# Performance work log

Measured on AMD Instinct MI355X. Metric: run time of the kernel, lower is better.

The kernel has to match this reference:

```python
import jax, jax.numpy as jnp
import numpy as np

T, IO, H, M = 8192, 32, 256, 4  # timesteps, io_width, hidden_width, max ponder steps
EPS = 0.01  # ACT halting epsilon


def setup_inputs() -> dict:
    key = jax.random.key(0)
    ks = jax.random.split(key, 8)
    sc = 0.05
    return {
        "x": jax.random.normal(ks[0], (T, IO), jnp.float32),
        "h0": jnp.zeros((H,), jnp.float32),                       # act1_h initial state
        "Wp": jax.random.normal(ks[1], (H, IO), jnp.float32) * sc,  # input_processing Linear
        "bp": jnp.zeros((H,), jnp.float32),
        "Wx": jax.random.normal(ks[2], (H, H + 1), jnp.float32) * sc,  # ACT cell input weights (+1 first-step flag)
        "Ws": jax.random.normal(ks[3], (H, H), jnp.float32) * sc,      # ACT cell recurrent weights
        "b": jnp.zeros((H,), jnp.float32),
        "wh": jax.random.normal(ks[4], (H,), jnp.float32) * sc,        # halting unit
        "bh": jnp.float32(1.0),
        "Wo": jax.random.normal(ks[5], (IO, H), jnp.float32) * sc,     # ACT output projection
        "bo": jnp.zeros((IO,), jnp.float32),
    }


def reference(x, h0, Wp, bp, Wx, Ws, b, wh, bh, Wo, bo):
    # Faithful translation: per-timestep loop (lax.scan) over the sequence; each step
    # runs input_processing then an ACT (Graves) ponder loop with max M=4 steps.
    # io_noise is identity in eval mode. attention_beam_width=1 => line == current point.
    T_ = x.shape[0]

    def step(carry, x_t):
        h, pc = carry
        lin1 = Wp @ x_t + bp  # [H]
        s = h
        cum = jnp.float32(0.0)
        acc_s = jnp.zeros_like(h)
        acc_y = jnp.zeros_like(bo)
        n_up = jnp.float32(0.0)
        rem = jnp.float32(0.0)
        still = jnp.bool_(True)
        for n in range(M):  # fixed small ponder loop, masked ACT halting
            flag = jnp.full((1,), 1.0 if n == 0 else 0.0, lin1.dtype)
            inp = jnp.concatenate([lin1, flag])  # [H+1]
            s = jnp.tanh(Wx @ inp + Ws @ s + b)
            p = jax.nn.sigmoid(wh @ s + bh)
            halt = (cum + p > 1.0 - EPS) | (n == M - 1)
            w = jnp.where(still, jnp.where(halt, 1.0 - cum, p), 0.0)
            acc_s = acc_s + w * s
            acc_y = acc_y + w * (Wo @ s + bo)
            rem = rem + jnp.where(still & halt, 1.0 - cum, 0.0)
            n_up = n_up + jnp.where(still, 1.0, 0.0)
            cum = cum + w
            still = still & jnp.logical_not(halt)
        ponder = n_up + rem  # N(t) + R(t)
        pc = (pc + ponder) / jnp.float32(T_)  # matches the in-loop division in the original forward
        return (acc_s, pc), acc_y

    (_, pc), ys = jax.lax.scan(step, (h0, jnp.float32(0.0)), x)
    return ys, pc
```

## Files before the change

kernel.cpp:

```cpp
#include <hip/hip_runtime.h>


#define T_  8192
#define IO_ 32
#define H_  256

template<int CTRL>
__device__ __forceinline__ float dpp_addf(float x) {
    int xi = __builtin_bit_cast(int, x);
    int d = __builtin_amdgcn_update_dpp(xi, xi, CTRL, 0xF, 0xF, false);
    return x + __builtin_bit_cast(float, d);
}

__global__ void k_prep(const float* __restrict__ Wx,
                       const float* __restrict__ Wp,
                       const float* __restrict__ bp,
                       const float* __restrict__ b,
                       float* __restrict__ WxpT, float* __restrict__ cvec) {
    int h = blockIdx.x;
    int t = threadIdx.x;
    __shared__ float wxrow[H_];
    for (int j = t; j < H_; j += 64) wxrow[j] = Wx[h * (H_ + 1) + j];
    __syncthreads();
    if (t < IO_) {
        float acc = 0.0f;
        for (int j = 0; j < H_; ++j) acc += wxrow[j] * Wp[j * IO_ + t];
        WxpT[t * H_ + h] = acc;
    } else if (t == IO_) {
        float acc = b[h];
        for (int j = 0; j < H_; ++j) acc += wxrow[j] * bp[j];
        cvec[h] = acc;
    }
}

__global__ void k_u(const float* __restrict__ x,
                    const float* __restrict__ WxpT,
                    const float* __restrict__ cvec,
                    float* __restrict__ U) {
    int t0 = blockIdx.x * 8;
    int tid = threadIdx.x;
    __shared__ float xsf[8 * IO_];
    xsf[tid] = x[(size_t)t0 * IO_ + tid];
    __syncthreads();
    int h = tid;
    float base = cvec[h];
    for (int tt = 0; tt < 8; ++tt) {
        float acc = base;
        #pragma unroll
        for (int io = 0; io < IO_; ++io)
            acc += WxpT[io * H_ + h] * xsf[tt * IO_ + io];
        U[(size_t)(t0 + tt) * H_ + h] = acc;
    }
}

__global__ __launch_bounds__(512, 2) void act_chain(
    const float* __restrict__ Ws,
    const float* __restrict__ Wx,
    const float* __restrict__ wh,
    const float* __restrict__ bh1,
    const float* __restrict__ h0,
    float* __restrict__ UAcc,
    float* __restrict__ cumArr,
    float* __restrict__ pc_out)
{
    __shared__ __align__(16) float sbuf[2][288];
    __shared__ __align__(16) float plds[2][8];

    const int tid = threadIdx.x;
    const int w   = tid >> 6;
    const int l   = tid & 63;
    const int rg  = l >> 3;
    const int c   = l & 7;
    const int rowbase = w * 32 + rg * 4;

    float4 wq[4][8];
    #pragma unroll
    for (int r = 0; r < 4; ++r) {
        const float4* src = (const float4*)(Ws + (size_t)(rowbase + r) * H_ + c * 32);
        #pragma unroll
        for (int k = 0; k < 8; ++k) wq[r][k] = src[k];
    }

    float wl4[4], whv4[4];
    #pragma unroll
    for (int r = 0; r < 4; ++r) {
        wl4[r]  = Wx[(size_t)(rowbase + r) * (H_ + 1) + H_];
        whv4[r] = wh[rowbase + r];
    }
    const float bhf = bh1[0];
    const float thresh = 1.0f - 0.01f;

    if (tid < H_) sbuf[0][(tid >> 5) * 36 + (tid & 31)] = h0[tid];
    __syncthreads();

    int cur = 0, pp = 0;
    float pc = 0.0f;

    #pragma unroll 1
    for (int tg = 0; tg < T_ / 4; ++tg) {
        float4 un[4];
        #pragma unroll
        for (int k = 0; k < 4; ++k)
            un[k] = *(const float4*)(UAcc + (size_t)(tg * 4 + k) * H_ + rowbase);

        float4 av[4];
        float  cu4[4];

        #pragma unroll
        for (int k = 0; k < 4; ++k) {
            const float u0 = un[k].x, u1 = un[k].y, u2 = un[k].z, u3 = un[k].w;

            float accs[4] = {0.f, 0.f, 0.f, 0.f};
            float cum = 0.0f, nup = 0.0f, remt = 0.0f;
            float sn[4];

            #pragma unroll 1
            for (int n = 0; n < 4; ++n) {
                const float4* sp = (const float4*)(&sbuf[cur][c * 36]);
                float4 sv[8];
                #pragma unroll
                for (int q = 0; q < 8; ++q) sv[q] = sp[q];

                float y[4];
                #pragma unroll
                for (int r = 0; r < 4; ++r) {
                    float a = 0.0f;
                    #pragma unroll
                    for (int q = 0; q < 8; ++q) {
                        a += wq[r][q].x * sv[q].x;
                        a += wq[r][q].y * sv[q].y;
                        a += wq[r][q].z * sv[q].z;
                        a += wq[r][q].w * sv[q].w;
                    }
                    a = dpp_addf<0xB1>(a);
                    a = dpp_addf<0x4E>(a);
                    a = dpp_addf<0x141>(a);
                    y[r] = a;
                }

                float part = 0.0f;
                float uu[4] = {u0, u1, u2, u3};
                #pragma unroll
                for (int r = 0; r < 4; ++r) {
                    float yy = y[r] + uu[r] + ((n == 0) ? wl4[r] : 0.0f);
                    float e = __expf(2.0f * yy);
                    sn[r] = 1.0f - 2.0f * __builtin_amdgcn_rcpf(e + 1.0f);
                    part += whv4[r] * sn[r];
                }

                int nxt = cur ^ 1;
                if (c == 0)
                    *(float4*)(&sbuf[nxt][w * 36 + rg * 4]) =
                        make_float4(sn[0], sn[1], sn[2], sn[3]);

                part = dpp_addf<0x128>(part);
                part = dpp_addf<0x142>(part);
                part = dpp_addf<0x143>(part);
                if (l == 63) plds[pp][w] = part;
                __syncthreads();

                float4 pa = *(const float4*)(&plds[pp][0]);
                float4 pb = *(const float4*)(&plds[pp][4]);
                float dot = ((pa.x + pa.y) + (pa.z + pa.w)) +
                            ((pb.x + pb.y) + (pb.z + pb.w));
                pp ^= 1;
                float p = __builtin_amdgcn_rcpf(1.0f + __expf(-(dot + bhf)));
                bool halt = (cum + p > thresh) || (n == 3);
                float hw = 1.0f - cum;
                float wn = halt ? hw : p;
                #pragma unroll
                for (int r = 0; r < 4; ++r) accs[r] += wn * sn[r];
                nup += 1.0f;
                cum += wn;
                if (halt) { remt = hw; break; }
                cur = nxt;
            }

            pc = (pc + nup + remt) * (1.0f / (float)T_);

            int hb = cur ^ 1;
            av[k] = make_float4(accs[0], accs[1], accs[2], accs[3]);
            cu4[k] = cum;
            if (c == 0)
                *(float4*)(&sbuf[hb][w * 36 + rg * 4]) = av[k];
            cur = hb;
            __syncthreads();
        }

        if (c == 0) {
            #pragma unroll
            for (int k = 0; k < 4; ++k)
                *(float4*)(UAcc + (size_t)(tg * 4 + k) * H_ + rowbase) = av[k];
        }
        if (tid == 0) {
            #pragma unroll
            for (int k = 0; k < 4; ++k) cumArr[tg * 4 + k] = cu4[k];
        }
    }
    if (tid == 0) pc_out[0] = pc;
}

__global__ void k_out(const float* __restrict__ AccS,
                      const float* __restrict__ Wo,
                      const float* __restrict__ bo,
                      const float* __restrict__ cumArr,
                      float* __restrict__ ys) {
    int t0 = blockIdx.x * 8;
    int tid = threadIdx.x;
    __shared__ float wo[IO_ * 257];
    __shared__ float as[8 * 260];
    for (int i = tid; i < IO_ * H_; i += 256) {
        int o = i / H_, h = i % H_;
        wo[o * 257 + h] = Wo[i];
    }
    for (int i = tid; i < 8 * H_; i += 256) {
        int tt = i / H_, h = i % H_;
        as[tt * 260 + h] = AccS[(size_t)t0 * H_ + i];
    }
    __syncthreads();
    int tt = tid >> 5, o = tid & 31;
    float acc = cumArr[t0 + tt] * bo[o];
    #pragma unroll 4
    for (int h = 0; h < H_; ++h) acc += wo[o * 257 + h] * as[tt * 260 + h];
    ys[(size_t)(t0 + tt) * IO_ + o] = acc;
}

extern "C" void kernel_launch(void* const* d_in, const int* in_sizes, int n_in,
                              void* d_out, int out_size, void* d_ws, size_t ws_size,
                              hipStream_t stream) {
    const float* x  = (const float*)d_in[0];
    const float* h0 = (const float*)d_in[1];
    const float* Wp = (const float*)d_in[2];
    const float* bp = (const float*)d_in[3];
    const float* Wx = (const float*)d_in[4];
    const float* Ws = (const float*)d_in[5];
    const float* b  = (const float*)d_in[6];
    const float* wh = (const float*)d_in[7];
    const float* bh = (const float*)d_in[8];
    const float* Wo = (const float*)d_in[9];
    const float* bo = (const float*)d_in[10];
    float* out = (float*)d_out;

    char* ws = (char*)d_ws;
    float* WxpT = (float*)ws;
    float* cvec = (float*)(ws + 32768);
    float* cumA = (float*)(ws + 33792);
    float* UAcc = (float*)(ws + 66560);

    k_prep<<<H_, 64, 0, stream>>>(Wx, Wp, bp, b, WxpT, cvec);
    k_u<<<T_ / 8, 256, 0, stream>>>(x, WxpT, cvec, UAcc);
    act_chain<<<1, 512, 0, stream>>>(Ws, Wx, wh, bh, h0, UAcc, cumA,
                                     out + (size_t)T_ * IO_);
    k_out<<<T_ / 8, 256, 0, stream>>>(UAcc, Wo, bo, cumA, out);
}
```

Before: 14.75 ms.

## Remap recurrent matvec to 2 rows x 4 column chunks with packed FP32 FMAs

Reworks the work split of the serial ACT chain kernel: each lane now owns 2 rows and a 64-column chunk (4 lanes per row group) instead of 4 rows and a 32-column chunk. The dot products use 2-wide float vectors so the compiler can emit packed FMA instructions. The cross-lane reduction shrinks to two DPP steps, while the halting-unit reduction gains one. The shared state buffer layout is changed to match. The tanh and sigmoid now call exp2 directly with prescaled constants. The aim is to shorten the per-ponder-step latency of the single-block recurrence, at the cost of longer per-lane accumulation chains and a different LDS read pattern.

```diff
diff --git a/kernel.cpp b/kernel.cpp
--- a/kernel.cpp
+++ b/kernel.cpp
@@ -4,6 +4,8 @@
 #define T_  8192
 #define IO_ 32
 #define H_  256
+
+typedef __attribute__((ext_vector_type(2))) float v2f;
 
 template<int CTRL>
 __device__ __forceinline__ float dpp_addf(float x) {
@@ -63,34 +65,41 @@
     float* __restrict__ cumArr,
     float* __restrict__ pc_out)
 {
-    __shared__ __align__(16) float sbuf[2][288];
+    __shared__ __align__(16) float sbuf[2][4 * 68];
     __shared__ __align__(16) float plds[2][8];
 
     const int tid = threadIdx.x;
     const int w   = tid >> 6;
     const int l   = tid & 63;
-    const int rg  = l >> 3;
-    const int c   = l & 7;
-    const int rowbase = w * 32 + rg * 4;
-
-    float4 wq[4][8];
+    const int rg  = l >> 2;
+    const int c   = l & 3;
+    const int rowbase = w * 32 + rg * 2;
+    const int schunk  = rowbase >> 6;
+    const int soff    = rowbase & 63;
+
+    v2f wt[2][32];
     #pragma unroll
-    for (int r = 0; r < 4; ++r) {
-        const float4* src = (const float4*)(Ws + (size_t)(rowbase + r) * H_ + c * 32);
-        #pragma unroll
-        for (int k = 0; k < 8; ++k) wq[r][k] = src[k];
-    }
-
-    float wl4[4], whv4[4];
-    #pragma unroll
-    for (int r = 0; r < 4; ++r) {
-        wl4[r]  = Wx[(size_t)(rowbase + r) * (H_ + 1) + H_];
-        whv4[r] = wh[rowbase + r];
-    }
+    for (int r = 0; r < 2; ++r) {
+        const float4* src = (const float4*)(Ws + (size_t)(rowbase + r) * H_ + c * 64);
+        #pragma unroll
+        for (int q = 0; q < 16; ++q) {
+            float4 f = src[q];
+            wt[r][2 * q]     = (v2f){f.x, f.y};
+            wt[r][2 * q + 1] = (v2f){f.z, f.w};
+        }
+    }
+
+    v2f wl2, whv2;
+    wl2.x  = Wx[(size_t)rowbase * (H_ + 1) + H_];
+    wl2.y  = Wx[(size_t)(rowbase + 1) * (H_ + 1) + H_];
+    whv2.x = wh[rowbase];
+    whv2.y = wh[rowbase + 1];
     const float bhf = bh1[0];
     const float thresh = 1.0f - 0.01f;
-
-    if (tid < H_) sbuf[0][(tid >> 5) * 36 + (tid & 31)] = h0[tid];
+    const float L2E  = 1.4426950408889634f;
+    const float L2E2 = 2.8853900817779268f;
+
+    if (tid < H_) sbuf[0][(tid >> 6) * 68 + (tid & 63)] = h0[tid];
     __syncthreads();
 
     int cur = 0, pp = 0;
@@ -98,61 +107,56 @@
 
     #pragma unroll 1
     for (int tg = 0; tg < T_ / 4; ++tg) {
-        float4 un[4];
+        v2f un[4];
         #pragma unroll
         for (int k = 0; k < 4; ++k)
-            un[k] = *(const float4*)(UAcc + (size_t)(tg * 4 + k) * H_ + rowbase);
-
-        float4 av[4];
-        float  cu4[4];
+            un[k] = *(const v2f*)(UAcc + (size_t)(tg * 4 + k) * H_ + rowbase);
+
+        v2f   av[4];
+        float cu4[4];
 
         #pragma unroll
         for (int k = 0; k < 4; ++k) {
-            const float u0 = un[k].x, u1 = un[k].y, u2 = un[k].z, u3 = un[k].w;
-
-            float accs[4] = {0.f, 0.f, 0.f, 0.f};
+            const v2f uu1 = un[k];
+            const v2f uu0 = uu1 + wl2;
+
+            v2f accs = {0.f, 0.f};
             float cum = 0.0f, nup = 0.0f, remt = 0.0f;
-            float sn[4];
+            float sn0, sn1;
 
             #pragma unroll 1
             for (int n = 0; n < 4; ++n) {
-                const float4* sp = (const float4*)(&sbuf[cur][c * 36]);
-                float4 sv[8];
+                v2f acc0 = {0.f, 0.f}, acc1 = {0.f, 0.f};
+                const float4* sp = (const float4*)(&sbuf[cur][c * 68]);
                 #pragma unroll
-                for (int q = 0; q < 8; ++q) sv[q] = sp[q];
-
-                float y[4];
-                #pragma unroll
-                for (int r = 0; r < 4; ++r) {
-                    float a = 0.0f;
-                    #pragma unroll
-                    for (int q = 0; q < 8; ++q) {
-                        a += wq[r][q].x * sv[q].x;
-                        a += wq[r][q].y * sv[q].y;
-                        a += wq[r][q].z * sv[q].z;
-                        a += wq[r][q].w * sv[q].w;
-                    }
-                    a = dpp_addf<0xB1>(a);
-                    a = dpp_addf<0x4E>(a);
-                    a = dpp_addf<0x141>(a);
-                    y[r] = a;
+                for (int q = 0; q < 16; ++q) {
+                    float4 f = sp[q];
+                    v2f sa = (v2f){f.x, f.y};
+                    v2f sb = (v2f){f.z, f.w};
+                    acc0 = acc0 + wt[0][2 * q] * sa;
+                    acc0 = acc0 + wt[0][2 * q + 1] * sb;
+                    acc1 = acc1 + wt[1][2 * q] * sa;
+                    acc1 = acc1 + wt[1][2 * q + 1] * sb;
                 }
-
-                float part = 0.0f;
-                float uu[4] = {u0, u1, u2, u3};
-                #pragma unroll
-                for (int r = 0; r < 4; ++r) {
-                    float yy = y[r] + uu[r] + ((n == 0) ? wl4[r] : 0.0f);
-                    float e = __expf(2.0f * yy);
-                    sn[r] = 1.0f - 2.0f * __builtin_amdgcn_rcpf(e + 1.0f);
-                    part += whv4[r] * sn[r];
-                }
+                float y0 = acc0.x + acc0.y;
+                float y1 = acc1.x + acc1.y;
+                y0 = dpp_addf<0xB1>(y0); y0 = dpp_addf<0x4E>(y0);
+                y1 = dpp_addf<0xB1>(y1); y1 = dpp_addf<0x4E>(y1);
+
+                v2f uu = (n == 0) ? uu0 : uu1;
+                float yy0 = y0 + uu.x;
+                float yy1 = y1 + uu.y;
+                float e0 = __builtin_amdgcn_exp2f(yy0 * L2E2);
+                float e1 = __builtin_amdgcn_exp2f(yy1 * L2E2);
+                sn0 = __builtin_fmaf(-2.0f, __builtin_amdgcn_rcpf(e0 + 1.0f), 1.0f);
+                sn1 = __builtin_fmaf(-2.0f, __builtin_amdgcn_rcpf(e1 + 1.0f), 1.0f);
 
                 int nxt = cur ^ 1;
                 if (c == 0)
-                    *(float4*)(&sbuf[nxt][w * 36 + rg * 4]) =
-                        make_float4(sn[0], sn[1], sn[2], sn[3]);
-
+                    *(v2f*)(&sbuf[nxt][schunk * 68 + soff]) = (v2f){sn0, sn1};
+
+                float part = __builtin_fmaf(whv2.x, sn0, whv2.y * sn1);
+                part = dpp_addf<0x124>(part);
                 part = dpp_addf<0x128>(part);
                 part = dpp_addf<0x142>(part);
                 part = dpp_addf<0x143>(part);
@@ -164,12 +168,12 @@
                 float dot = ((pa.x + pa.y) + (pa.z + pa.w)) +
                             ((pb.x + pb.y) + (pb.z + pb.w));
                 pp ^= 1;
-                float p = __builtin_amdgcn_rcpf(1.0f + __expf(-(dot + bhf)));
+                float p = __builtin_amdgcn_rcpf(
+                    1.0f + __builtin_amdgcn_exp2f(-(dot + bhf) * L2E));
                 bool halt = (cum + p > thresh) || (n == 3);
                 float hw = 1.0f - cum;
                 float wn = halt ? hw : p;
-                #pragma unroll
-                for (int r = 0; r < 4; ++r) accs[r] += wn * sn[r];
+                accs = accs + wn * (v2f){sn0, sn1};
                 nup += 1.0f;
                 cum += wn;
                 if (halt) { remt = hw; break; }
@@ -179,10 +183,10 @@
             pc = (pc + nup + remt) * (1.0f / (float)T_);
 
             int hb = cur ^ 1;
-            av[k] = make_float4(accs[0], accs[1], accs[2], accs[3]);
+            av[k]  = accs;
             cu4[k] = cum;
             if (c == 0)
-                *(float4*)(&sbuf[hb][w * 36 + rg * 4]) = av[k];
+                *(v2f*)(&sbuf[hb][schunk * 68 + soff]) = accs;
             cur = hb;
             __syncthreads();
         }
@@ -190,7 +194,7 @@
         if (c == 0) {
             #pragma unroll
             for (int k = 0; k < 4; ++k)
-                *(float4*)(UAcc + (size_t)(tg * 4 + k) * H_ + rowbase) = av[k];
+                *(v2f*)(UAcc + (size_t)(tg * 4 + k) * H_ + rowbase) = av[k];
         }
         if (tid == 0) {
             #pragma unroll
```

Result: faster. 12.10 ms (-17.9%).
